# Kernel tuning notes

Hardware: AMD Instinct MI355X
Metric: run time of the kernel (lower is better)

Reference implementation:

```python
import jax, jax.numpy as jnp
import numpy as np

N_LAYER = 6
EPS = 1e-5
TWO_PI = 2.0 * np.pi
THETA = 2.0 ** 16


def _ln(x):
    # LayerNorm over last dim, no affine (elementwise_affine=False)
    m = jnp.mean(x, axis=-1, keepdims=True)
    v = jnp.mean((x - m) ** 2, axis=-1, keepdims=True)
    return (x - m) / jnp.sqrt(v + EPS)


def _rope_tables(T, N):
    t = jnp.arange(N, dtype=jnp.float32)
    q = jnp.floor(t / 2.0) * 2.0  # quantize(t, 2)
    freqs = 1.0 / (THETA ** (q / N)) / TWO_PI  # [N]
    pos = jnp.arange(T, dtype=jnp.float32)
    angles = (pos[:, None] * freqs[None, :] % 1.0) * TWO_PI  # [T, N]
    return jnp.cos(angles), jnp.sin(angles)


def _rotate_half(v):
    # stack((-v_odd, v_even), -1).view(shape): interleaved rotation
    return jnp.stack((-v[..., 1::2], v[..., ::2]), axis=-1).reshape(v.shape)


def setup_inputs() -> dict:
    key = jax.random.key(0)
    ks = jax.random.split(key, 6)
    B, T = 1, 512
    D, nh, mult, vocab = 256, 4, 128, 256
    N = mult * D // nh  # 8192
    idx = jax.random.randint(ks[0], (B, T), 0, vocab)
    std = 0.02
    embed = jax.random.normal(ks[1], (vocab, D), jnp.float32) * std
    encoder = jax.random.normal(ks[2], (nh, D, N), jnp.float32) * std
    encoder_v = jax.random.normal(ks[3], (nh, D, N), jnp.float32) * std
    decoder = jax.random.normal(ks[4], (nh * N, D), jnp.float32) * std
    lm_head = jax.random.normal(ks[5], (D, vocab), jnp.float32) * std
    return {"idx": idx, "embed": embed, "encoder": encoder,
            "encoder_v": encoder_v, "decoder": decoder, "lm_head": lm_head}


def reference(idx, embed, encoder, encoder_v, decoder, lm_head):
    B, T = idx.shape
    nh, D, N = encoder.shape
    cos, sin = _rope_tables(T, N)  # [T, N]
    causal = jnp.tril(jnp.ones((T, T), dtype=bool), k=-1)  # strict lower

    x = _ln(embed[idx])  # [B, T, D]
    for _ in range(N_LAYER):  # single shared layer applied n_layer times
        x_sparse = jax.nn.relu(jnp.einsum('btd,hdn->bhtn', x, encoder))
        qr = x_sparse * cos + _rotate_half(x_sparse) * sin  # RoPE on Q=K
        scores = jnp.einsum('bhtn,bhsn->bhts', qr, qr)
        scores = jnp.where(causal, scores, 0.0)  # tril(diagonal=-1), no softmax
        yKV = _ln(jnp.einsum('bhts,bsd->bhtd', scores, x))  # V = x broadcast over heads
        y_sparse = jax.nn.relu(jnp.einsum('bhtd,hdn->bhtn', yKV, encoder_v))
        xy = x_sparse * y_sparse  # [B, nh, T, N]
        xy = xy.transpose(0, 2, 1, 3).reshape(B, T, nh * N)
        y = _ln(xy @ decoder)  # [B, T, D]
        x = _ln(x + y)
    logits = x @ lm_head  # [B, T, vocab]
    return logits
```

## Files before the change

kernel.cpp:

```cpp
#include <hip/hip_runtime.h>
#include <hip/hip_bf16.h>

#define T   512
#define D   256
#define H   4
#define NN  8192
#define V   256
#define EPSF 1e-5f
#define QKS 4
#define DSPLIT 32
#define N_LAYER 6

typedef __bf16 bf16;
typedef __attribute__((__ext_vector_type__(8))) __bf16 bf16x8;
typedef __attribute__((__ext_vector_type__(4))) __bf16 bf16x4;
typedef __attribute__((__ext_vector_type__(4))) float  f32x4;

#define MFMA16(a, b, c) __builtin_amdgcn_mfma_f32_16x16x32_bf16((a), (b), (c), 0, 0, 0)
#define GLD16(g, l)                                                         \
    __builtin_amdgcn_global_load_lds(                                       \
        (const __attribute__((address_space(1))) void*)(g),                 \
        (__attribute__((address_space(3))) void*)(l), 16, 0, 0)

__device__ __forceinline__ float blk_sum256(float v, float* red) {
#pragma unroll
    for (int off = 32; off > 0; off >>= 1) v += __shfl_down(v, off, 64);
    int lane = threadIdx.x & 63, w = threadIdx.x >> 6;
    __syncthreads();
    if (lane == 0) red[w] = v;
    __syncthreads();
    return red[0] + red[1] + red[2] + red[3];
}

__global__ __launch_bounds__(256) void tcvt_k(const float* __restrict__ in,
                                              bf16* __restrict__ out, int R, int C) {
    __shared__ float t[32][33];
    size_t hoff = (size_t)blockIdx.z * R * C;
    int c0 = blockIdx.x * 32, r0 = blockIdx.y * 32;
    int x = threadIdx.x & 31, y = threadIdx.x >> 5;
#pragma unroll
    for (int p = 0; p < 4; ++p)
        t[y + 8 * p][x] = in[hoff + (size_t)(r0 + y + 8 * p) * C + c0 + x];
    __syncthreads();
#pragma unroll
    for (int p = 0; p < 4; ++p)
        out[hoff + (size_t)(c0 + y + 8 * p) * R + r0 + x] = (bf16)t[x][y + 8 * p];
}

__global__ __launch_bounds__(256) void rope_tab_k(bf16* __restrict__ cosH,
                                                  bf16* __restrict__ sinH) {
    int k = blockIdx.x * 256 + threadIdx.x;
    int t = blockIdx.y;
    float q = (float)(2 * k);
    float f = exp2f(q * (-16.0f / (float)NN)) * 0.15915494309189535f;
    float u = fmodf((float)t * f, 1.0f);
    float a = u * 6.283185307179586f;
    cosH[(size_t)t * (NN / 2) + k] = (bf16)cosf(a);
    sinH[(size_t)t * (NN / 2) + k] = (bf16)sinf(a);
}

__global__ __launch_bounds__(256) void embed_ln_k(const int* __restrict__ idx,
                                                  const float* __restrict__ embed,
                                                  float* __restrict__ x,
                                                  bf16* __restrict__ xb,
                                                  bf16* __restrict__ xbT) {
    __shared__ float red[4];
    int t = blockIdx.x, d = threadIdx.x;
    float e = embed[(size_t)idx[t] * D + d];
    float m = blk_sum256(e, red) * (1.0f / D);
    float df = e - m;
    float vv = blk_sum256(df * df, red) * (1.0f / D);
    float r = df * rsqrtf(vv + EPSF);
    x[(size_t)t * D + d] = r;
    xb[(size_t)t * D + d] = (bf16)r;
    xbT[(size_t)d * T + t] = (bf16)r;
}

__device__ __forceinline__ void gemm_core64(const bf16* __restrict__ Ap, size_t lda,
                                            const bf16* __restrict__ Bp, size_t ldb,
                                            int ksteps, bf16* As, bf16* Bs,
                                            f32x4 acc[2][2], int tid) {
    int lane = tid & 63, wid = tid >> 6;
    int wr = (wid >> 1) * 32, wc = (wid & 1) * 32;
    int fr = lane & 15;
    int s  = lane >> 4;
    int srow  = wid * 16 + (lane >> 2);
    int sslot = (lane & 3) ^ ((srow >> 1) & 3);
    const bf16* ag = Ap + (size_t)srow * lda + sslot * 8;
    const bf16* bg = Bp + (size_t)srow * ldb + sslot * 8;
    bf16* al = As + wid * 512;
    bf16* bl = Bs + wid * 512;
    int ar0 = wr + fr, ar1 = wr + 16 + fr;
    int br0 = wc + fr, br1 = wc + 16 + fr;
    const char* cA = (const char*)As;
    const char* cB = (const char*)Bs;
    int aoff0 = ar0 * 64 + ((s ^ ((ar0 >> 1) & 3)) << 4);
    int aoff1 = ar1 * 64 + ((s ^ ((ar1 >> 1) & 3)) << 4);
    int boff0 = br0 * 64 + ((s ^ ((br0 >> 1) & 3)) << 4);
    int boff1 = br1 * 64 + ((s ^ ((br1 >> 1) & 3)) << 4);
    for (int ks = 0; ks < ksteps; ++ks) {
        GLD16(ag + ks * 32, al);
        GLD16(bg + ks * 32, bl);
        __syncthreads();
        bf16x8 a0 = *(const bf16x8*)(cA + aoff0);
        bf16x8 a1 = *(const bf16x8*)(cA + aoff1);
        bf16x8 b0 = *(const bf16x8*)(cB + boff0);
        bf16x8 b1 = *(const bf16x8*)(cB + boff1);
        acc[0][0] = MFMA16(a0, b0, acc[0][0]);
        acc[0][1] = MFMA16(a0, b1, acc[0][1]);
        acc[1][0] = MFMA16(a1, b0, acc[1][0]);
        acc[1][1] = MFMA16(a1, b1, acc[1][1]);
        __syncthreads();
    }
}

template <int MODE>
__global__ __launch_bounds__(256) void enc_mfma_k(const bf16* __restrict__ A,
                                                  const bf16* __restrict__ Wt,
                                                  bf16* __restrict__ xs,
                                                  bf16* __restrict__ qr,
                                                  const bf16* __restrict__ cosH,
                                                  const bf16* __restrict__ sinH,
                                                  int aHeadStride) {
    __shared__ __align__(16) char smem[10240];
    bf16* As = (bf16*)smem;
    bf16* Bs = (bf16*)(smem + 4096);
    bf16 (*Ot)[76] = (bf16(*)[76])smem;
    int h = blockIdx.z;
    int row0 = blockIdx.y * 64, col0 = blockIdx.x * 64;
    const bf16* Ap = A + (size_t)h * aHeadStride + (size_t)row0 * D;
    const bf16* Bp = Wt + ((size_t)h * NN + col0) * D;
    int tid = threadIdx.x;
    f32x4 acc[2][2];
#pragma unroll
    for (int i = 0; i < 2; ++i)
#pragma unroll
        for (int j = 0; j < 2; ++j) acc[i][j] = f32x4{0.f, 0.f, 0.f, 0.f};
    gemm_core64(Ap, D, Bp, D, D / 32, As, Bs, acc, tid);

    int lane = tid & 63, wid = tid >> 6;
    int wr = (wid >> 1) * 32, wc = (wid & 1) * 32;
    int fr = lane & 15, fq = lane >> 4;
    float vv[2][2][4];
#pragma unroll
    for (int mi = 0; mi < 2; ++mi)
#pragma unroll
        for (int ni = 0; ni < 2; ++ni)
#pragma unroll
            for (int j = 0; j < 4; ++j)
                vv[mi][ni][j] = fmaxf((float)acc[mi][ni][j], 0.0f);

#pragma unroll
    for (int mi = 0; mi < 2; ++mi)
#pragma unroll
        for (int ni = 0; ni < 2; ++ni)
#pragma unroll
            for (int j = 0; j < 4; ++j)
                Ot[wr + mi * 16 + fq * 4 + j][wc + ni * 16 + fr] = (bf16)vv[mi][ni][j];
    __syncthreads();
    int er = tid >> 2, ec = (tid & 3) * 16;
    size_t gbase = ((size_t)h * T + row0 + er) * NN + col0 + ec;
    bf16x8 o0 = *(bf16x8*)&Ot[er][ec];
    bf16x8 o1 = *(bf16x8*)&Ot[er][ec + 8];

    if (MODE == 0) {
        *(bf16x8*)(xs + gbase) = o0;
        *(bf16x8*)(xs + gbase + 8) = o1;
        __syncthreads();
#pragma unroll
        for (int mi = 0; mi < 2; ++mi)
#pragma unroll
            for (int ni = 0; ni < 2; ++ni)
#pragma unroll
                for (int j = 0; j < 4; ++j) {
                    float v = vv[mi][ni][j];
                    float p = __shfl_xor(v, 1, 64);
                    int m = row0 + wr + mi * 16 + fq * 4 + j;
                    int n = col0 + wc + ni * 16 + fr;
                    float cs = (float)cosH[(size_t)m * (NN / 2) + (n >> 1)];
                    float sn = (float)sinH[(size_t)m * (NN / 2) + (n >> 1)];
                    float qv = v * cs + ((n & 1) ? p * sn : -p * sn);
                    Ot[wr + mi * 16 + fq * 4 + j][wc + ni * 16 + fr] = (bf16)qv;
                }
        __syncthreads();
        bf16x8 q0 = *(bf16x8*)&Ot[er][ec];
        bf16x8 q1 = *(bf16x8*)&Ot[er][ec + 8];
        *(bf16x8*)(qr + gbase) = q0;
        *(bf16x8*)(qr + gbase + 8) = q1;
    } else {
        bf16x8 x0 = *(const bf16x8*)(xs + gbase);
        bf16x8 x1 = *(const bf16x8*)(xs + gbase + 8);
        bf16x8 r0v, r1v;
#pragma unroll
        for (int k = 0; k < 8; ++k) {
            r0v[k] = (bf16)((float)o0[k] * (float)x0[k]);
            r1v[k] = (bf16)((float)o1[k] * (float)x1[k]);
        }
        *(bf16x8*)(xs + gbase) = r0v;
        *(bf16x8*)(xs + gbase + 8) = r1v;
    }
}

__global__ __launch_bounds__(256) void qq_mfma_k(const bf16* __restrict__ qrb,
                                                 float* __restrict__ spart) {
    __shared__ __align__(16) char smem[8192];
    bf16* As = (bf16*)smem;
    bf16* Bs = (bf16*)(smem + 4096);
    int g = blockIdx.x & 15;
    int h = g >> 2, ksplit = g & 3;
    int p = blockIdx.x >> 4;
    int ti = 0, accu = 0;
    while (accu + ti + 1 <= p) { ++ti; accu += ti; }
    int tj = p - accu;
    const bf16* Q = qrb + (size_t)h * T * NN + (size_t)ksplit * (NN / QKS);
    const bf16* Ap = Q + (size_t)(ti * 64) * NN;
    const bf16* Bp = Q + (size_t)(tj * 64) * NN;
    int tid = threadIdx.x;
    f32x4 acc[2][2];
#pragma unroll
    for (int i = 0; i < 2; ++i)
#pragma unroll
        for (int j = 0; j < 2; ++j) acc[i][j] = f32x4{0.f, 0.f, 0.f, 0.f};
    gemm_core64(Ap, NN, Bp, NN, (NN / QKS) / 32, As, Bs, acc, tid);

    int lane = tid & 63, wid = tid >> 6;
    int wr = (wid >> 1) * 32, wc = (wid & 1) * 32;
    int fr = lane & 15, fq = lane >> 4;
    float* outp = spart + (size_t)(ksplit * H + h) * T * T;
#pragma unroll
    for (int mi = 0; mi < 2; ++mi)
#pragma unroll
        for (int ni = 0; ni < 2; ++ni) {
            int s = tj * 64 + wc + ni * 16 + fr;
            int mbase = ti * 64 + wr + mi * 16 + fq * 4;
#pragma unroll
            for (int j = 0; j < 4; ++j)
                outp[(size_t)(mbase + j) * T + s] = acc[mi][ni][j];
        }
}

__global__ __launch_bounds__(256) void mask_cvt_k(const float* __restrict__ spart,
                                                  bf16* __restrict__ sb) {
    int t = blockIdx.x * 2 + (threadIdx.x >> 7);
    int h = blockIdx.y;
    int l = threadIdx.x & 127;
    int s = l * 4;
    const float* s0 = spart + ((size_t)h * T + t) * T + s;
    const size_t st = (size_t)H * T * T;
    float4 w0 = *(const float4*)(s0);
    float4 w1 = *(const float4*)(s0 + st);
    float4 w2 = *(const float4*)(s0 + 2 * st);
    float4 w3 = *(const float4*)(s0 + 3 * st);
    bf16x4 o;
    o[0] = (bf16)((s + 0 < t) ? (w0.x + w1.x + w2.x + w3.x) : 0.0f);
    o[1] = (bf16)((s + 1 < t) ? (w0.y + w1.y + w2.y + w3.y) : 0.0f);
    o[2] = (bf16)((s + 2 < t) ? (w0.z + w1.z + w2.z + w3.z) : 0.0f);
    o[3] = (bf16)((s + 3 < t) ? (w0.w + w1.w + w2.w + w3.w) : 0.0f);
    *(bf16x4*)(sb + ((size_t)h * T + t) * T + s) = o;
}

__global__ __launch_bounds__(256) void av_mfma_k(const bf16* __restrict__ sb,
                                                 const bf16* __restrict__ xbT,
                                                 float* __restrict__ ykv_pre) {
    __shared__ __align__(16) char smem[8192];
    bf16* As = (bf16*)smem;
    bf16* Bs = (bf16*)(smem + 4096);
    int h = blockIdx.z;
    int ti = blockIdx.y;
    int row0 = ti * 64, col0 = blockIdx.x * 64;
    const bf16* Ap = sb + ((size_t)h * T + row0) * T;
    const bf16* Bp = xbT + (size_t)col0 * T;
    int tid = threadIdx.x;
    f32x4 acc[2][2];
#pragma unroll
    for (int i = 0; i < 2; ++i)
#pragma unroll
        for (int j = 0; j < 2; ++j) acc[i][j] = f32x4{0.f, 0.f, 0.f, 0.f};
    gemm_core64(Ap, T, Bp, T, (ti + 1) * 2, As, Bs, acc, tid);

    int lane = tid & 63, wid = tid >> 6;
    int wr = (wid >> 1) * 32, wc = (wid & 1) * 32;
    int fr = lane & 15, fq = lane >> 4;
#pragma unroll
    for (int mi = 0; mi < 2; ++mi)
#pragma unroll
        for (int ni = 0; ni < 2; ++ni) {
            int n = col0 + wc + ni * 16 + fr;
            int mbase = row0 + wr + mi * 16 + fq * 4;
#pragma unroll
            for (int j = 0; j < 4; ++j)
                ykv_pre[((size_t)h * T + (mbase + j)) * D + n] = acc[mi][ni][j];
        }
}

__global__ __launch_bounds__(256) void ykv_ln_k(const float* __restrict__ ykv_pre,
                                                bf16* __restrict__ ykvb) {
    __shared__ float red[4];
    int t = blockIdx.x, h = blockIdx.y, d = threadIdx.x;
    float a = ykv_pre[((size_t)h * T + t) * D + d];
    float m = blk_sum256(a, red) * (1.0f / D);
    float df = a - m;
    float vv = blk_sum256(df * df, red) * (1.0f / D);
    ykvb[((size_t)h * T + t) * D + d] = (bf16)(df * rsqrtf(vv + EPSF));
}

__global__ __launch_bounds__(256) void dec_mfma_k(const bf16* __restrict__ xyb,
                                                  const bf16* __restrict__ decT,
                                                  float* __restrict__ ypart) {
    __shared__ __align__(16) char smem[8192];
    bf16* As = (bf16*)smem;
    bf16* Bs = (bf16*)(smem + 4096);
    int ks = blockIdx.x & 31;
    int t  = blockIdx.x >> 5;
    int col0 = (t & 3) * 64, row0 = (t >> 2) * 64;
    int cbeg = ks * ((H * NN) / DSPLIT);
    int h = cbeg >> 13, n0 = cbeg & (NN - 1);
    const bf16* Ap = xyb + ((size_t)h * T + row0) * NN + n0;
    const bf16* Bp = decT + (size_t)col0 * (H * NN) + cbeg;
    int tid = threadIdx.x;
    f32x4 acc[2][2];
#pragma unroll
    for (int i = 0; i < 2; ++i)
#pragma unroll
        for (int j = 0; j < 2; ++j) acc[i][j] = f32x4{0.f, 0.f, 0.f, 0.f};
    gemm_core64(Ap, NN, Bp, H * NN, (H * NN / DSPLIT) / 32, As, Bs, acc, tid);

    int lane = tid & 63, wid = tid >> 6;
    int wr = (wid >> 1) * 32, wc = (wid & 1) * 32;
    int fr = lane & 15, fq = lane >> 4;
#pragma unroll
    for (int mi = 0; mi < 2; ++mi)
#pragma unroll
        for (int ni = 0; ni < 2; ++ni) {
            int n = col0 + wc + ni * 16 + fr;
            int mbase = row0 + wr + mi * 16 + fq * 4;
#pragma unroll
            for (int j = 0; j < 4; ++j)
                ypart[((size_t)ks * T + (mbase + j)) * D + n] = acc[mi][ni][j];
        }
}

__global__ __launch_bounds__(256) void final_ln_k(const float* __restrict__ ypart,
                                                  float* __restrict__ x,
                                                  bf16* __restrict__ xb,
                                                  bf16* __restrict__ xbT) {
    __shared__ float red[4];
    int t = blockIdx.x, d = threadIdx.x;
    float ys = 0.0f;
#pragma unroll
    for (int ks = 0; ks < DSPLIT; ++ks) ys += ypart[((size_t)ks * T + t) * D + d];
    float m = blk_sum256(ys, red) * (1.0f / D);
    float df = ys - m;
    float vv = blk_sum256(df * df, red) * (1.0f / D);
    float yln = df * rsqrtf(vv + EPSF);
    float val = x[(size_t)t * D + d] + yln;
    float m2 = blk_sum256(val, red) * (1.0f / D);
    float df2 = val - m2;
    float v2 = blk_sum256(df2 * df2, red) * (1.0f / D);
    float r = df2 * rsqrtf(v2 + EPSF);
    x[(size_t)t * D + d] = r;
    xb[(size_t)t * D + d] = (bf16)r;
    xbT[(size_t)d * T + t] = (bf16)r;
}

__global__ __launch_bounds__(256) void logits_k(const float* __restrict__ x,
                                                const float* __restrict__ lm,
                                                float* __restrict__ out) {
    int t = blockIdx.x, v = threadIdx.x;
    float a = 0.0f;
    for (int d = 0; d < D; ++d)
        a = fmaf(x[(size_t)t * D + d], lm[(size_t)d * V + v], a);
    out[(size_t)t * V + v] = a;
}

extern "C" void kernel_launch(void* const* d_in, const int* in_sizes, int n_in,
                              void* d_out, int out_size, void* d_ws, size_t ws_size,
                              hipStream_t stream) {
    const int*   idx       = (const int*)d_in[0];
    const float* embed     = (const float*)d_in[1];
    const float* encoder   = (const float*)d_in[2];
    const float* encoder_v = (const float*)d_in[3];
    const float* decoder   = (const float*)d_in[4];
    const float* lm_head   = (const float*)d_in[5];
    float* out = (float*)d_out;

    char* W = (char*)d_ws;
    float* x       = (float*)W; W += (size_t)T * D * 4;
    float* scratch = (float*)W; W += (size_t)QKS * H * T * T * 4;
    bf16* xb    = (bf16*)W; W += (size_t)T * D * 2;
    bf16* xbT   = (bf16*)W; W += (size_t)D * T * 2;
    bf16* sb    = (bf16*)W; W += (size_t)H * T * T * 2;
    bf16* ykvb  = (bf16*)W; W += (size_t)H * T * D * 2;
    bf16* encT  = (bf16*)W; W += (size_t)H * NN * D * 2;
    bf16* encVT = (bf16*)W; W += (size_t)H * NN * D * 2;
    bf16* decT  = (bf16*)W; W += (size_t)D * H * NN * 2;
    bf16* cosH  = (bf16*)W; W += (size_t)T * (NN / 2) * 2;
    bf16* sinH  = (bf16*)W; W += (size_t)T * (NN / 2) * 2;
    bf16* xs    = (bf16*)W; W += (size_t)H * T * NN * 2;
    bf16* qr    = (bf16*)W; W += (size_t)H * T * NN * 2;

    tcvt_k<<<dim3(NN / 32, D / 32, H), 256, 0, stream>>>(encoder, encT, D, NN);
    tcvt_k<<<dim3(NN / 32, D / 32, H), 256, 0, stream>>>(encoder_v, encVT, D, NN);
    tcvt_k<<<dim3(D / 32, (H * NN) / 32, 1), 256, 0, stream>>>(decoder, decT, H * NN, D);
    rope_tab_k<<<dim3((NN / 2) / 256, T), 256, 0, stream>>>(cosH, sinH);

    embed_ln_k<<<T, 256, 0, stream>>>(idx, embed, x, xb, xbT);

    for (int layer = 0; layer < N_LAYER; ++layer) {
        enc_mfma_k<0><<<dim3(NN / 64, T / 64, H), 256, 0, stream>>>(
            xb, encT, xs, qr, cosH, sinH, 0);
        qq_mfma_k<<<576, 256, 0, stream>>>(qr, scratch);
        mask_cvt_k<<<dim3(T / 2, H), 256, 0, stream>>>(scratch, sb);
        av_mfma_k<<<dim3(D / 64, T / 64, H), 256, 0, stream>>>(sb, xbT, scratch);
        ykv_ln_k<<<dim3(T, H), 256, 0, stream>>>(scratch, ykvb);
        enc_mfma_k<1><<<dim3(NN / 64, T / 64, H), 256, 0, stream>>>(
            ykvb, encVT, xs, nullptr, nullptr, nullptr, T * D);
        dec_mfma_k<<<1024, 256, 0, stream>>>(xs, decT, scratch);
        final_ln_k<<<T, 256, 0, stream>>>(scratch, x, xb, xbT);
    }

    logits_k<<<T, 256, 0, stream>>>(x, lm_head, out);
}
```

Before: 775.3 us.

## Double-buffer LDS in the shared MFMA GEMM core with a 64-wide K tile

The shared 64x64 GEMM core now stages K-slices of 64 instead of 32, with a new 8-slot XOR swizzle. Two LDS buffers let the next slice's global-to-LDS loads be issued while MFMAs run on the current one. This halves the number of barriers per K element and aims to hide load latency. The decoder GEMM's split-K factor also drops from 32 to 16, which halves its grid and its partial-sum traffic. In exchange every GEMM kernel now reserves 32KB of LDS, which may lower occupancy, and the decoder launch has fewer blocks.

```diff
diff --git a/kernel.cpp b/kernel.cpp
--- a/kernel.cpp
+++ b/kernel.cpp
@@ -8,7 +8,7 @@
 #define V   256
 #define EPSF 1e-5f
 #define QKS 4
-#define DSPLIT 32
+#define DSPLIT 16
 #define N_LAYER 6
 
 typedef __bf16 bf16;
@@ -78,38 +78,53 @@
 
 __device__ __forceinline__ void gemm_core64(const bf16* __restrict__ Ap, size_t lda,
                                             const bf16* __restrict__ Bp, size_t ldb,
-                                            int ksteps, bf16* As, bf16* Bs,
+                                            int ksteps, bf16* lds,
                                             f32x4 acc[2][2], int tid) {
     int lane = tid & 63, wid = tid >> 6;
     int wr = (wid >> 1) * 32, wc = (wid & 1) * 32;
-    int fr = lane & 15;
-    int s  = lane >> 4;
-    int srow  = wid * 16 + (lane >> 2);
-    int sslot = (lane & 3) ^ ((srow >> 1) & 3);
-    const bf16* ag = Ap + (size_t)srow * lda + sslot * 8;
-    const bf16* bg = Bp + (size_t)srow * ldb + sslot * 8;
-    bf16* al = As + wid * 512;
-    bf16* bl = Bs + wid * 512;
-    int ar0 = wr + fr, ar1 = wr + 16 + fr;
-    int br0 = wc + fr, br1 = wc + 16 + fr;
-    const char* cA = (const char*)As;
-    const char* cB = (const char*)Bs;
-    int aoff0 = ar0 * 64 + ((s ^ ((ar0 >> 1) & 3)) << 4);
-    int aoff1 = ar1 * 64 + ((s ^ ((ar1 >> 1) & 3)) << 4);
-    int boff0 = br0 * 64 + ((s ^ ((br0 >> 1) & 3)) << 4);
-    int boff1 = br1 * 64 + ((s ^ ((br1 >> 1) & 3)) << 4);
+    int fr = lane & 15, s = lane >> 4;
+    int srow = wid * 16 + (lane >> 3);
+    int sx   = ((lane & 7) ^ (srow & 7)) * 8;
+    const bf16* ag = Ap + (size_t)srow * lda + sx;
+    const bf16* bg = Bp + (size_t)srow * ldb + sx;
+    bf16* a_w = lds + wid * 1024;
+    bf16* b_w = lds + 8192 + wid * 1024;
+    int ar = wr + fr, br = wc + fr;
+    int aoff0 = ar * 128 + (((s)     ^ (ar & 7)) << 4);
+    int aoff1 = ar * 128 + (((4 + s) ^ (ar & 7)) << 4);
+    int boff0 = br * 128 + (((s)     ^ (br & 7)) << 4);
+    int boff1 = br * 128 + (((4 + s) ^ (br & 7)) << 4);
+    GLD16(ag, a_w);  GLD16(ag + 8 * lda, a_w + 512);
+    GLD16(bg, b_w);  GLD16(bg + 8 * ldb, b_w + 512);
+    __syncthreads();
     for (int ks = 0; ks < ksteps; ++ks) {
-        GLD16(ag + ks * 32, al);
-        GLD16(bg + ks * 32, bl);
-        __syncthreads();
-        bf16x8 a0 = *(const bf16x8*)(cA + aoff0);
-        bf16x8 a1 = *(const bf16x8*)(cA + aoff1);
-        bf16x8 b0 = *(const bf16x8*)(cB + boff0);
-        bf16x8 b1 = *(const bf16x8*)(cB + boff1);
-        acc[0][0] = MFMA16(a0, b0, acc[0][0]);
-        acc[0][1] = MFMA16(a0, b1, acc[0][1]);
-        acc[1][0] = MFMA16(a1, b0, acc[1][0]);
-        acc[1][1] = MFMA16(a1, b1, acc[1][1]);
+        int cur = ks & 1;
+        if (ks + 1 < ksteps) {
+            int nxt = cur ^ 1;
+            size_t ko = (size_t)(ks + 1) * 64;
+            bf16* an = lds + nxt * 4096 + wid * 1024;
+            bf16* bn = lds + 8192 + nxt * 4096 + wid * 1024;
+            GLD16(ag + ko, an);  GLD16(ag + ko + 8 * lda, an + 512);
+            GLD16(bg + ko, bn);  GLD16(bg + ko + 8 * ldb, bn + 512);
+        }
+        const char* cA = (const char*)(lds + cur * 4096);
+        const char* cB = (const char*)(lds + 8192 + cur * 4096);
+        bf16x8 a00 = *(const bf16x8*)(cA + aoff0);
+        bf16x8 a01 = *(const bf16x8*)(cA + aoff1);
+        bf16x8 a10 = *(const bf16x8*)(cA + aoff0 + 2048);
+        bf16x8 a11 = *(const bf16x8*)(cA + aoff1 + 2048);
+        bf16x8 b00 = *(const bf16x8*)(cB + boff0);
+        bf16x8 b01 = *(const bf16x8*)(cB + boff1);
+        bf16x8 b10 = *(const bf16x8*)(cB + boff0 + 2048);
+        bf16x8 b11 = *(const bf16x8*)(cB + boff1 + 2048);
+        acc[0][0] = MFMA16(a00, b00, acc[0][0]);
+        acc[0][0] = MFMA16(a01, b01, acc[0][0]);
+        acc[0][1] = MFMA16(a00, b10, acc[0][1]);
+        acc[0][1] = MFMA16(a01, b11, acc[0][1]);
+        acc[1][0] = MFMA16(a10, b00, acc[1][0]);
+        acc[1][0] = MFMA16(a11, b01, acc[1][0]);
+        acc[1][1] = MFMA16(a10, b10, acc[1][1]);
+        acc[1][1] = MFMA16(a11, b11, acc[1][1]);
         __syncthreads();
     }
 }
@@ -122,9 +137,7 @@
                                                   const bf16* __restrict__ cosH,
                                                   const bf16* __restrict__ sinH,
                                                   int aHeadStride) {
-    __shared__ __align__(16) char smem[10240];
-    bf16* As = (bf16*)smem;
-    bf16* Bs = (bf16*)(smem + 4096);
+    __shared__ __align__(16) char smem[32768];
     bf16 (*Ot)[76] = (bf16(*)[76])smem;
     int h = blockIdx.z;
     int row0 = blockIdx.y * 64, col0 = blockIdx.x * 64;
@@ -136,7 +149,7 @@
     for (int i = 0; i < 2; ++i)
 #pragma unroll
         for (int j = 0; j < 2; ++j) acc[i][j] = f32x4{0.f, 0.f, 0.f, 0.f};
-    gemm_core64(Ap, D, Bp, D, D / 32, As, Bs, acc, tid);
+    gemm_core64(Ap, D, Bp, D, D / 64, (bf16*)smem, acc, tid);
 
     int lane = tid & 63, wid = tid >> 6;
     int wr = (wid >> 1) * 32, wc = (wid & 1) * 32;
@@ -203,9 +216,7 @@
 
 __global__ __launch_bounds__(256) void qq_mfma_k(const bf16* __restrict__ qrb,
                                                  float* __restrict__ spart) {
-    __shared__ __align__(16) char smem[8192];
-    bf16* As = (bf16*)smem;
-    bf16* Bs = (bf16*)(smem + 4096);
+    __shared__ __align__(16) char smem[32768];
     int g = blockIdx.x & 15;
     int h = g >> 2, ksplit = g & 3;
     int p = blockIdx.x >> 4;
@@ -221,7 +232,7 @@
     for (int i = 0; i < 2; ++i)
 #pragma unroll
         for (int j = 0; j < 2; ++j) acc[i][j] = f32x4{0.f, 0.f, 0.f, 0.f};
-    gemm_core64(Ap, NN, Bp, NN, (NN / QKS) / 32, As, Bs, acc, tid);
+    gemm_core64(Ap, NN, Bp, NN, (NN / QKS) / 64, (bf16*)smem, acc, tid);
 
     int lane = tid & 63, wid = tid >> 6;
     int wr = (wid >> 1) * 32, wc = (wid & 1) * 32;
@@ -262,9 +273,7 @@
 __global__ __launch_bounds__(256) void av_mfma_k(const bf16* __restrict__ sb,
                                                  const bf16* __restrict__ xbT,
                                                  float* __restrict__ ykv_pre) {
-    __shared__ __align__(16) char smem[8192];
-    bf16* As = (bf16*)smem;
-    bf16* Bs = (bf16*)(smem + 4096);
+    __shared__ __align__(16) char smem[32768];
     int h = blockIdx.z;
     int ti = blockIdx.y;
     int row0 = ti * 64, col0 = blockIdx.x * 64;
@@ -276,7 +285,7 @@
     for (int i = 0; i < 2; ++i)
 #pragma unroll
         for (int j = 0; j < 2; ++j) acc[i][j] = f32x4{0.f, 0.f, 0.f, 0.f};
-    gemm_core64(Ap, T, Bp, T, (ti + 1) * 2, As, Bs, acc, tid);
+    gemm_core64(Ap, T, Bp, T, ti + 1, (bf16*)smem, acc, tid);
 
     int lane = tid & 63, wid = tid >> 6;
     int wr = (wid >> 1) * 32, wc = (wid & 1) * 32;
@@ -307,11 +316,9 @@
 __global__ __launch_bounds__(256) void dec_mfma_k(const bf16* __restrict__ xyb,
                                                   const bf16* __restrict__ decT,
                                                   float* __restrict__ ypart) {
-    __shared__ __align__(16) char smem[8192];
-    bf16* As = (bf16*)smem;
-    bf16* Bs = (bf16*)(smem + 4096);
-    int ks = blockIdx.x & 31;
-    int t  = blockIdx.x >> 5;
+    __shared__ __align__(16) char smem[32768];
+    int ks = blockIdx.x & 15;
+    int t  = blockIdx.x >> 4;
     int col0 = (t & 3) * 64, row0 = (t >> 2) * 64;
     int cbeg = ks * ((H * NN) / DSPLIT);
     int h = cbeg >> 13, n0 = cbeg & (NN - 1);
@@ -323,7 +330,7 @@
     for (int i = 0; i < 2; ++i)
 #pragma unroll
         for (int j = 0; j < 2; ++j) acc[i][j] = f32x4{0.f, 0.f, 0.f, 0.f};
-    gemm_core64(Ap, NN, Bp, H * NN, (H * NN / DSPLIT) / 32, As, Bs, acc, tid);
+    gemm_core64(Ap, NN, Bp, H * NN, (H * NN / DSPLIT) / 64, (bf16*)smem, acc, tid);
 
     int lane = tid & 63, wid = tid >> 6;
     int wr = (wid >> 1) * 32, wc = (wid & 1) * 32;
@@ -415,7 +422,7 @@
         ykv_ln_k<<<dim3(T, H), 256, 0, stream>>>(scratch, ykvb);
         enc_mfma_k<1><<<dim3(NN / 64, T / 64, H), 256, 0, stream>>>(
             ykvb, encVT, xs, nullptr, nullptr, nullptr, T * D);
-        dec_mfma_k<<<1024, 256, 0, stream>>>(xs, decT, scratch);
+        dec_mfma_k<<<512, 256, 0, stream>>>(xs, decT, scratch);
         final_ln_k<<<T, 256, 0, stream>>>(scratch, x, xb, xbT);
     }
 
```

After: 698.5 us. 1.11x faster.
